# Optimization experiments

Hardware: AMD Instinct MI355X
Metric: run time of the kernel (lower is better)

Reference implementation:

```python
import jax, jax.numpy as jnp
import numpy as np

B, S, D_IN, D_INT, D_OUT, E, K_SYN = 2, 2048, 2048, 2048, 2048, 4, 512
GROUPS = D_INT // 8  # Conv1d groups

def setup_inputs() -> dict:
    key = jax.random.key(0)
    ks = jax.random.split(key, 20)
    n = lambda k, sh, std: jax.random.normal(k, sh, dtype=jnp.float32) * std
    d = {}
    d['x'] = jax.random.normal(ks[0], (B, S, D_IN), dtype=jnp.float32)
    d['syntax_ids'] = jax.random.randint(ks[1], (B, S), 0, K_SYN, dtype=jnp.int32)
    d['W_in'] = n(ks[2], (D_IN, D_INT), D_IN ** -0.5)
    d['b_in'] = jnp.zeros((D_INT,), jnp.float32)
    d['W_syn_emb'] = n(ks[3], (K_SYN, D_INT // 4), 0.02)
    d['W_syn'] = n(ks[4], (D_INT + D_INT // 4, D_INT), 0.02)
    d['b_syn'] = jnp.zeros((D_INT,), jnp.float32)
    d['W_gate'] = n(ks[5], (D_INT, 1), 0.02)
    d['b_gate'] = jnp.zeros((1,), jnp.float32)
    d['W_router'] = n(ks[6], (D_INT, E), 0.02)
    d['b_router'] = jnp.zeros((E,), jnp.float32)
    d['W_e1'] = n(ks[7], (E, D_INT, 2 * D_INT), 0.02)
    d['b_e1'] = jnp.zeros((E, 2 * D_INT), jnp.float32)
    d['W_e2'] = n(ks[8], (E, 2 * D_INT, D_INT), 0.02)
    d['b_e2'] = jnp.zeros((E, D_INT), jnp.float32)
    d['W_ctx'] = n(ks[9], (D_INT, D_INT), D_INT ** -0.5)
    d['b_ctx'] = jnp.zeros((D_INT,), jnp.float32)
    fan = 8 * 3 + 8 * 3
    lim = float(np.sqrt(6.0 / fan))
    d['conv_w'] = jax.random.uniform(ks[10], (D_INT, 8, 3), jnp.float32, -lim, lim)
    d['conv_b'] = jnp.zeros((D_INT,), jnp.float32)
    d['W_out'] = n(ks[11], (D_INT, D_OUT), D_INT ** -0.5)
    d['b_out'] = jnp.zeros((D_OUT,), jnp.float32)
    return d

def _forward(x, syntax_ids, W_in, b_in, W_syn_emb, W_syn, b_syn, W_gate, b_gate,
             W_router, b_router, W_e1, b_e1, W_e2, b_e2, W_ctx, b_ctx,
             conv_w, conv_b, W_out, b_out):
    # input projection + SiLU (dropout is identity in eval / p=0)
    h = jax.nn.silu(jnp.einsum('bsi,id->bsd', x, W_in) + b_in)
    # syntax-aware projection
    se = W_syn_emb[syntax_ids]                       # [B,S,D/4] gather
    h = jnp.einsum('bsc,cd->bsd', jnp.concatenate([h, se], axis=-1), W_syn) + b_syn
    # adaptive computation gate
    gate = jax.nn.sigmoid(jnp.einsum('bsd,do->bso', h, W_gate) + b_gate)
    h = h * gate
    # dense mixture-of-experts combine (softmax router weights)
    probs = jax.nn.softmax(jnp.einsum('bsd,de->bse', h, W_router) + b_router, axis=-1)
    eh = jax.nn.silu(jnp.einsum('bsd,edf->bsef', h, W_e1) + b_e1)   # [B,S,E,2D]
    eo = jnp.einsum('bsef,efd->bsed', eh, W_e2) + b_e2              # [B,S,E,D]
    h = h + jnp.einsum('bsed,bse->bsd', eo, probs)
    # code-specific: context linear + grouped Conv1d pattern extractor
    ctx = jnp.einsum('bsd,df->bsf', h, W_ctx) + b_ctx
    hc = jnp.transpose(h, (0, 2, 1))  # [B,D,S]
    pat = jax.lax.conv_general_dilated(
        hc, conv_w, window_strides=(1,), padding=((1, 1),),
        dimension_numbers=('NCH', 'OIH', 'NCH'), feature_group_count=GROUPS)
    pat = jnp.transpose(pat + conv_b[None, :, None], (0, 2, 1))
    h = h + ctx + pat
    out = jnp.einsum('bsd,do->bso', h, W_out) + b_out
    return out + x  # residual (input_dim == output_dim)

def reference(x, syntax_ids, W_in, b_in, W_syn_emb, W_syn, b_syn, W_gate, b_gate,
              W_router, b_router, W_e1, b_e1, W_e2, b_e2, W_ctx, b_ctx,
              conv_w, conv_b, W_out, b_out):
    return _forward(x, syntax_ids, W_in, b_in, W_syn_emb, W_syn, b_syn, W_gate,
                    b_gate, W_router, b_router, W_e1, b_e1, W_e2, b_e2,
                    W_ctx, b_ctx, conv_w, conv_b, W_out, b_out)
```

## Files before the change

kernel.cpp:

```cpp
#include <hip/hip_runtime.h>

typedef __attribute__((ext_vector_type(8))) short short8;
typedef __attribute__((ext_vector_type(4))) float floatx4;

#define BM 128
#define BN 128
#define BK 32

__device__ __forceinline__ float b2f(ushort us) {
    union { unsigned u; float f; } v; v.u = ((unsigned)us) << 16; return v.f;
}
__device__ __forceinline__ ushort f2b(float f) {
    union { float f; unsigned u; } v; v.f = f;
    unsigned r = (v.u + 0x7fffu + ((v.u >> 16) & 1u)) >> 16;
    return (ushort)r;
}
__device__ __forceinline__ float ldany(const void* p, long i, int bf) {
    return bf ? b2f(((const ushort*)p)[i]) : ((const float*)p)[i];
}
__device__ __forceinline__ void async16(const ushort* g, ushort* l) {
    __builtin_amdgcn_global_load_lds((const __attribute__((address_space(1))) void*)g,
                                     (__attribute__((address_space(3))) void*)l,
                                     16, 0, 0);
}

__global__ void detect_dtype(const unsigned* __restrict__ w, int* __restrict__ flag)
{
    if (threadIdx.x == 0 && blockIdx.x == 0) {
        int votes = 0;
        for (int i = 0; i < 256; i++) {
            unsigned e = (w[i] >> 7) & 0xFFu;
            if (e >= 112u && e <= 128u) votes++;
        }
        *flag = (votes >= 128) ? 1 : 0;
    }
}

__global__ __launch_bounds__(256) void transpose_any(
    const void* __restrict__ in, long in_off, ushort* __restrict__ out,
    int R, int C, const int* __restrict__ flag)
{
    __shared__ float tile[64][65];
    const int bf = *flag;
    const int t  = threadIdx.x;
    const long r0 = (long)blockIdx.y * 64;
    const long c0 = (long)blockIdx.x * 64;
    const int rl = t >> 4;
    const int cl = (t & 15) * 4;
    #pragma unroll
    for (int p = 0; p < 4; p++) {
        const int r = rl + p * 16;
        const long base = in_off + (r0 + r) * C + c0 + cl;
        if (bf) {
            ushort4 v = *(const ushort4*)((const ushort*)in + base);
            tile[r][cl + 0] = b2f(v.x); tile[r][cl + 1] = b2f(v.y);
            tile[r][cl + 2] = b2f(v.z); tile[r][cl + 3] = b2f(v.w);
        } else {
            float4 v = *(const float4*)((const float*)in + base);
            tile[r][cl + 0] = v.x; tile[r][cl + 1] = v.y;
            tile[r][cl + 2] = v.z; tile[r][cl + 3] = v.w;
        }
    }
    __syncthreads();
    #pragma unroll
    for (int p = 0; p < 4; p++) {
        const int oc = rl + p * 16;
        ushort4 v;
        v.x = f2b(tile[cl + 0][oc]); v.y = f2b(tile[cl + 1][oc]);
        v.z = f2b(tile[cl + 2][oc]); v.w = f2b(tile[cl + 3][oc]);
        *(ushort4*)(out + (c0 + oc) * R + r0 + cl) = v;
    }
}

__global__ void to_bf16_any(const void* __restrict__ in, ushort* __restrict__ out,
                            long n4, const int* __restrict__ flag)
{
    const long i = (long)blockIdx.x * blockDim.x + threadIdx.x;
    if (i >= n4) return;
    const int bf = *flag;
    ushort4 o;
    if (bf) {
        o = ((const ushort4*)in)[i];
    } else {
        float4 v = ((const float4*)in)[i];
        o.x = f2b(v.x); o.y = f2b(v.y); o.z = f2b(v.z); o.w = f2b(v.w);
    }
    ((ushort4*)out)[i] = o;
}

__global__ void f32_to_bf16_4(const float* __restrict__ in, ushort* __restrict__ out, long n4)
{
    const long i = (long)blockIdx.x * blockDim.x + threadIdx.x;
    if (i >= n4) return;
    float4 v = ((const float4*)in)[i];
    ushort4 o; o.x = f2b(v.x); o.y = f2b(v.y); o.z = f2b(v.z); o.w = f2b(v.w);
    ((ushort4*)out)[i] = o;
}

#define EPI_SILU   0
#define EPI_BIAS   1
#define EPI_EXPERT 2
#define EPI_CTX    3
#define EPI_OUT    4

template<int EPI>
__global__ __launch_bounds__(256, 2) void gemm_bt(
    const ushort* __restrict__ A, const ushort* __restrict__ Bt,
    int M, int N, int K,
    const void* __restrict__ bias, long bias_off,
    void* __restrict__ out, long ldo,
    float* __restrict__ hacc,
    const float* __restrict__ rowscale,
    const ushort* __restrict__ resid,
    const int* __restrict__ flag)
{
    __shared__ __align__(16) ushort As[BM * BK];
    __shared__ __align__(16) ushort Bs[BN * BK];

    const int tid  = threadIdx.x;
    const int lane = tid & 63;
    const int wv   = tid >> 6;
    const int wm   = wv & 1;
    const int wn   = wv >> 1;
    const long m0  = (long)blockIdx.y * BM;
    const long n0  = (long)blockIdx.x * BN;

    floatx4 acc[4][4] = {};

    const int sr = (lane >> 2);
    const int sk = (lane & 3) * 8;
    const ushort* Ag = A  + (m0 + wv * 32 + sr) * (long)K + sk;
    const ushort* Bg = Bt + (n0 + wv * 32 + sr) * (long)K + sk;
    ushort* Al = As + (wv * 32) * BK;
    ushort* Bl = Bs + (wv * 32) * BK;

    const int fr = lane & 15;
    const int q  = lane >> 4;
    const ushort* ApL = As + (wm * 64 + fr) * BK + q * 8;
    const ushort* BpL = Bs + (wn * 64 + fr) * BK + q * 8;

    for (int k0 = 0; k0 < K; k0 += BK) {
        __syncthreads();
        async16(Ag + k0,            Al);
        async16(Ag + 16L * K + k0,  Al + 16 * BK);
        async16(Bg + k0,            Bl);
        async16(Bg + 16L * K + k0,  Bl + 16 * BK);
        __syncthreads();
        short8 af[4], bfr[4];
        #pragma unroll
        for (int i = 0; i < 4; i++) af[i]  = *(const short8*)(ApL + i * 16 * BK);
        #pragma unroll
        for (int j = 0; j < 4; j++) bfr[j] = *(const short8*)(BpL + j * 16 * BK);
        #pragma unroll
        for (int i = 0; i < 4; i++)
            #pragma unroll
            for (int j = 0; j < 4; j++)
                acc[i][j] = __builtin_amdgcn_mfma_f32_16x16x32_bf16(
                                af[i], bfr[j], acc[i][j], 0, 0, 0);
    }

    const int bf = *flag;
    #pragma unroll
    for (int i = 0; i < 4; i++) {
        #pragma unroll
        for (int r = 0; r < 4; r++) {
            const long m = m0 + wm * 64 + i * 16 + q * 4 + r;
            #pragma unroll
            for (int j = 0; j < 4; j++) {
                const long n = n0 + wn * 64 + j * 16 + fr;
                float v = acc[i][j][r] + ldany(bias, bias_off + n, bf);
                if (EPI == EPI_SILU) {
                    v = v / (1.f + __expf(-v));
                    ((ushort*)out)[m * ldo + n] = f2b(v);
                } else if (EPI == EPI_BIAS) {
                    ((ushort*)out)[m * ldo + n] = f2b(v);
                } else if (EPI == EPI_EXPERT) {
                    hacc[m * (long)N + n] += rowscale[m * 4] * v;
                } else if (EPI == EPI_CTX) {
                    hacc[m * (long)N + n] += v;
                } else {
                    v += b2f(resid[m * (long)N + n]);
                    if (bf) ((ushort*)out)[m * ldo + n] = f2b(v);
                    else    ((float*)out)[m * ldo + n]  = v;
                }
            }
        }
    }
}

__global__ void gather_syn(const int* __restrict__ ids, const void* __restrict__ emb,
                           ushort* __restrict__ hA, const int* __restrict__ flag)
{
    const int bf = *flag;
    const long m = blockIdx.x;
    const int id = ids[m];
    const int j = threadIdx.x * 2;
    float a, b;
    if (bf) {
        ushort2 v = *(const ushort2*)((const ushort*)emb + (long)id * 512 + j);
        a = b2f(v.x); b = b2f(v.y);
    } else {
        float2 v = *(const float2*)((const float*)emb + (long)id * 512 + j);
        a = v.x; b = v.y;
    }
    ushort2 o; o.x = f2b(a); o.y = f2b(b);
    *(ushort2*)(hA + m * 2560 + 2048 + j) = o;
}

__global__ __launch_bounds__(256) void gate_router(
    ushort* __restrict__ h2, float* __restrict__ hacc, float* __restrict__ probs,
    const void* __restrict__ Wg, const void* __restrict__ bg,
    const void* __restrict__ Wr, const void* __restrict__ br,
    const int* __restrict__ flag)
{
    const int bf = *flag;
    const long m = blockIdx.x;
    const int t = threadIdx.x;
    const int lane = t & 63;
    const int wv = t >> 6;
    ushort* row = h2 + m * 2048;

    float sg = 0.f, s0 = 0.f, s1 = 0.f, s2 = 0.f, s3 = 0.f;
    for (int k = t; k < 2048; k += 256) {
        const float h = b2f(row[k]);
        sg += h * ldany(Wg, k, bf);
        float r0v, r1v, r2v, r3v;
        if (bf) {
            ushort4 v = *(const ushort4*)((const ushort*)Wr + (long)k * 4);
            r0v = b2f(v.x); r1v = b2f(v.y); r2v = b2f(v.z); r3v = b2f(v.w);
        } else {
            float4 v = *(const float4*)((const float*)Wr + (long)k * 4);
            r0v = v.x; r1v = v.y; r2v = v.z; r3v = v.w;
        }
        s0 += h * r0v; s1 += h * r1v; s2 += h * r2v; s3 += h * r3v;
    }
    #pragma unroll
    for (int off = 32; off > 0; off >>= 1) {
        sg += __shfl_down(sg, off);
        s0 += __shfl_down(s0, off);
        s1 += __shfl_down(s1, off);
        s2 += __shfl_down(s2, off);
        s3 += __shfl_down(s3, off);
    }
    __shared__ float red[4][5];
    __shared__ float gate_bc;
    if (lane == 0) {
        red[wv][0] = sg; red[wv][1] = s0; red[wv][2] = s1;
        red[wv][3] = s2; red[wv][4] = s3;
    }
    __syncthreads();
    if (t == 0) {
        float G = red[0][0] + red[1][0] + red[2][0] + red[3][0];
        float R[4];
        #pragma unroll
        for (int e = 0; e < 4; e++)
            R[e] = red[0][1 + e] + red[1][1 + e] + red[2][1 + e] + red[3][1 + e];
        const float gate = 1.f / (1.f + __expf(-(G + ldany(bg, 0, bf))));
        float lg[4], mx = -1e30f;
        #pragma unroll
        for (int e = 0; e < 4; e++) {
            lg[e] = gate * R[e] + ldany(br, e, bf);
            mx = fmaxf(mx, lg[e]);
        }
        float p[4], s = 0.f;
        #pragma unroll
        for (int e = 0; e < 4; e++) { p[e] = __expf(lg[e] - mx); s += p[e]; }
        #pragma unroll
        for (int e = 0; e < 4; e++) probs[m * 4 + e] = p[e] / s;
        gate_bc = gate;
    }
    __syncthreads();
    const float gate = gate_bc;
    for (int k = t; k < 2048; k += 256) {
        const float v = b2f(row[k]) * gate;
        row[k] = f2b(v);
        hacc[m * 2048 + k] = v;
    }
}

__global__ __launch_bounds__(256) void conv_combine(
    const ushort* __restrict__ h4, const float* __restrict__ hacc,
    const void* __restrict__ cw, const void* __restrict__ cb,
    ushort* __restrict__ h5, const int* __restrict__ flag)
{
    const int S = 2048, D = 2048;
    const int bf = *flag;
    const int b = blockIdx.z, g = blockIdx.y;
    const int s0 = blockIdx.x * 64;
    __shared__ float tile[66 * 8];
    const int t = threadIdx.x;
    for (int idx = t; idx < 66 * 8; idx += 256) {
        const int sl = idx >> 3, i = idx & 7;
        const int s = s0 + sl - 1;
        float v = 0.f;
        if (s >= 0 && s < S) v = b2f(h4[((long)b * S + s) * D + g * 8 + i]);
        tile[idx] = v;
    }
    __syncthreads();
    const int io = t & 7;
    const int c = g * 8 + io;
    float w[3][8];
    #pragma unroll
    for (int kk = 0; kk < 3; kk++)
        #pragma unroll
        for (int ii = 0; ii < 8; ii++)
            w[kk][ii] = ldany(cw, (long)c * 24 + ii * 3 + kk, bf);
    const float bc = ldany(cb, c, bf);
    #pragma unroll
    for (int p = 0; p < 2; p++) {
        const int sl = (t >> 3) + p * 32;
        float pat = 0.f;
        #pragma unroll
        for (int kk = 0; kk < 3; kk++)
            #pragma unroll
            for (int ii = 0; ii < 8; ii++)
                pat += tile[(sl + kk) * 8 + ii] * w[kk][ii];
        const long m = (long)b * S + s0 + sl;
        h5[m * D + c] = f2b(hacc[m * D + c] + bc + pat);
    }
}

extern "C" void kernel_launch(void* const* d_in, const int* in_sizes, int n_in,
                              void* d_out, int out_size, void* d_ws, size_t ws_size,
                              hipStream_t stream)
{
    (void)in_sizes; (void)n_in; (void)out_size; (void)ws_size;
    const void* x        = d_in[0];
    const int*  syn      = (const int*)d_in[1];
    const void* W_in     = d_in[2];
    const void* b_in     = d_in[3];
    const void* W_synemb = d_in[4];
    const void* W_syn    = d_in[5];
    const void* b_syn    = d_in[6];
    const void* W_gate   = d_in[7];
    const void* b_gate   = d_in[8];
    const void* W_router = d_in[9];
    const void* b_router = d_in[10];
    const void* W_e1     = d_in[11];
    const void* b_e1     = d_in[12];
    const void* W_e2     = d_in[13];
    const void* b_e2     = d_in[14];
    const void* W_ctx    = d_in[15];
    const void* b_ctx    = d_in[16];
    const void* conv_w   = d_in[17];
    const void* conv_b   = d_in[18];
    const void* W_out    = d_in[19];
    const void* b_out    = d_in[20];

    char* ws = (char*)d_ws;
    int*    flag  = (int*)ws;
    ushort* WT    = (ushort*)(ws + 256);
    ushort* xb    = (ushort*)(ws + 16777472);
    ushort* hA    = (ushort*)(ws + 33554688);
    ushort* eh    = (ushort*)(ws + 16777472);
    ushort* h23   = (ushort*)(ws + 54526208);
    float*  probs = (float*)(ws + 71303424);
    float*  hacc  = (float*)(ws + 71368960);
    const int M = 4096;
    dim3 blk(256);

    detect_dtype<<<dim3(1), dim3(64), 0, stream>>>((const unsigned*)W_in, flag);
    to_bf16_any<<<dim3(8192), blk, 0, stream>>>(x, xb, 2097152L, flag);

    transpose_any<<<dim3(32, 32), blk, 0, stream>>>(W_in, 0, WT, 2048, 2048, flag);
    gemm_bt<EPI_SILU><<<dim3(16, 32), blk, 0, stream>>>(
        xb, WT, M, 2048, 2048, b_in, 0, hA, 2560, nullptr, nullptr, nullptr, flag);
    gather_syn<<<dim3(4096), blk, 0, stream>>>(syn, W_synemb, hA, flag);
    transpose_any<<<dim3(32, 40), blk, 0, stream>>>(W_syn, 0, WT, 2560, 2048, flag);
    gemm_bt<EPI_BIAS><<<dim3(16, 32), blk, 0, stream>>>(
        hA, WT, M, 2048, 2560, b_syn, 0, h23, 2048, nullptr, nullptr, nullptr, flag);
    gate_router<<<dim3(4096), blk, 0, stream>>>(
        h23, hacc, probs, W_gate, b_gate, W_router, b_router, flag);
    for (int e = 0; e < 4; e++) {
        transpose_any<<<dim3(64, 32), blk, 0, stream>>>(
            W_e1, (long)e * 8388608, WT, 2048, 4096, flag);
        gemm_bt<EPI_SILU><<<dim3(32, 32), blk, 0, stream>>>(
            h23, WT, M, 4096, 2048, b_e1, (long)e * 4096, eh, 4096,
            nullptr, nullptr, nullptr, flag);
        transpose_any<<<dim3(32, 64), blk, 0, stream>>>(
            W_e2, (long)e * 8388608, WT, 4096, 2048, flag);
        gemm_bt<EPI_EXPERT><<<dim3(16, 32), blk, 0, stream>>>(
            eh, WT, M, 2048, 4096, b_e2, (long)e * 2048, nullptr, 0,
            hacc, probs + e, nullptr, flag);
    }
    to_bf16_any<<<dim3(8192), blk, 0, stream>>>(x, xb, 2097152L, flag);
    f32_to_bf16_4<<<dim3(8192), blk, 0, stream>>>(hacc, h23, 2097152L);
    transpose_any<<<dim3(32, 32), blk, 0, stream>>>(W_ctx, 0, WT, 2048, 2048, flag);
    gemm_bt<EPI_CTX><<<dim3(16, 32), blk, 0, stream>>>(
        h23, WT, M, 2048, 2048, b_ctx, 0, nullptr, 0, hacc, nullptr, nullptr, flag);
    conv_combine<<<dim3(32, 256, 2), blk, 0, stream>>>(
        h23, hacc, conv_w, conv_b, hA, flag);
    transpose_any<<<dim3(32, 32), blk, 0, stream>>>(W_out, 0, WT, 2048, 2048, flag);
    gemm_bt<EPI_OUT><<<dim3(16, 32), blk, 0, stream>>>(
        hA, WT, M, 2048, 2048, b_out, 0, d_out, 2048, nullptr, nullptr, xb, flag);
}
```

Baseline: 1.562 ms.

## Replace GEMM with 8-wave double-buffered ping-pong MFMA kernel using swizzled LDS

```diff
diff --git a/kernel.cpp b/kernel.cpp
--- a/kernel.cpp
+++ b/kernel.cpp
@@ -2,10 +2,6 @@
 
 typedef __attribute__((ext_vector_type(8))) short short8;
 typedef __attribute__((ext_vector_type(4))) float floatx4;
-
-#define BM 128
-#define BN 128
-#define BK 32
 
 __device__ __forceinline__ float b2f(ushort us) {
     union { unsigned u; float f; } v; v.u = ((unsigned)us) << 16; return v.f;
@@ -103,8 +99,74 @@
 #define EPI_CTX    3
 #define EPI_OUT    4
 
-template<int EPI>
-__global__ __launch_bounds__(256, 2) void gemm_bt(
+#define BAR()        __builtin_amdgcn_s_barrier()
+#define WAIT_LGKM0() asm volatile("s_waitcnt lgkmcnt(0)" ::: "memory")
+#define WAIT_VM6()   asm volatile("s_waitcnt vmcnt(6)" ::: "memory")
+#define WAIT_VM5()   asm volatile("s_waitcnt vmcnt(5)" ::: "memory")
+#define WAIT_VM0()   asm volatile("s_waitcnt vmcnt(0)" ::: "memory")
+
+#define STAGE_A(BUF, H, KT) do {                                               \
+    const long _k0 = (long)(KT) << 6;                                          \
+    _Pragma("unroll")                                                          \
+    for (int _i = 0; _i < AINSTR; ++_i) {                                      \
+        const int _gi   = w + _i * 8;                                          \
+        const int _s    = _gi / AHALF_GRP;                                     \
+        const int _wg   = _gi % AHALF_GRP;                                     \
+        const int _row0 = _s * (BM / 2) + (H) * (BM / 4) + _wg * 8;            \
+        const int _grow = _row0 + (lane >> 3);                                 \
+        async16(A + (m0 + _grow) * (long)K + _k0 +                             \
+                    (((lane & 7) ^ (_grow & 7)) << 3),                         \
+                smem + (BUF) * BUFU + _row0 * 64);                             \
+    } } while (0)
+
+#define STAGE_B(BUF, H, KT) do {                                               \
+    const long _k0 = (long)(KT) << 6;                                          \
+    _Pragma("unroll")                                                          \
+    for (int _i = 0; _i < 2; ++_i) {                                           \
+        const int _gi   = w * 2 + _i;                                          \
+        const int _row0 = (_gi >> 2) * 64 + (H) * 32 + (_gi & 3) * 8;          \
+        const int _grow = _row0 + (lane >> 3);                                 \
+        async16(Bt + (n0 + _grow) * (long)K + _k0 +                            \
+                     (((lane & 7) ^ (_grow & 7)) << 3),                        \
+                smem + (BUF) * BUFU + BM * 64 + _row0 * 64);                   \
+    } } while (0)
+
+#define LOAD_A(BUF, MH) do {                                                   \
+    _Pragma("unroll")                                                          \
+    for (int _m = 0; _m < MF / 2; ++_m) {                                      \
+        const int _row = wm * (BM / 2) + ((MH) * (MF / 2) + _m) * 16 + fr;     \
+        _Pragma("unroll")                                                      \
+        for (int _ks = 0; _ks < 2; ++_ks)                                      \
+            a[_m][_ks] = *(const short8*)(smem + (BUF) * BUFU + _row * 64 +    \
+                                          (((_ks * 4 + q) ^ (_row & 7)) << 3));\
+    } } while (0)
+
+#define LOAD_B(BUF, NH, BREG) do {                                             \
+    _Pragma("unroll")                                                          \
+    for (int _n = 0; _n < 2; ++_n) {                                           \
+        const int _row = wn * 64 + ((NH) * 2 + _n) * 16 + fr;                  \
+        _Pragma("unroll")                                                      \
+        for (int _ks = 0; _ks < 2; ++_ks)                                      \
+            BREG[_n][_ks] = *(const short8*)(smem + (BUF) * BUFU + BM * 64 +   \
+                                             _row * 64 +                       \
+                                          (((_ks * 4 + q) ^ (_row & 7)) << 3));\
+    } } while (0)
+
+#define MMA(MH, NH, BREG) do {                                                 \
+    _Pragma("unroll")                                                          \
+    for (int _m = 0; _m < MF / 2; ++_m)                                        \
+    _Pragma("unroll")                                                          \
+    for (int _n = 0; _n < 2; ++_n)                                             \
+    _Pragma("unroll")                                                          \
+    for (int _ks = 0; _ks < 2; ++_ks)                                          \
+        acc[(MH) * (MF / 2) + _m][(NH) * 2 + _n] =                             \
+            __builtin_amdgcn_mfma_f32_16x16x32_bf16(                           \
+                a[_m][_ks], BREG[_n][_ks],                                     \
+                acc[(MH) * (MF / 2) + _m][(NH) * 2 + _n], 0, 0, 0);            \
+    } while (0)
+
+template<int EPI, int MF>
+__global__ __launch_bounds__(512, 2) void gemm8(
     const ushort* __restrict__ A, const ushort* __restrict__ Bt,
     int M, int N, int K,
     const void* __restrict__ bias, long bias_off,
@@ -114,59 +176,69 @@
     const ushort* __restrict__ resid,
     const int* __restrict__ flag)
 {
-    __shared__ __align__(16) ushort As[BM * BK];
-    __shared__ __align__(16) ushort Bs[BN * BK];
+    constexpr int BM        = MF * 32;
+    constexpr int AHALF_GRP = BM / 32;
+    constexpr int AINSTR    = BM / 128;
+    constexpr int BUFU      = (BM + 256) * 64;
+    extern __shared__ ushort smem[];
 
     const int tid  = threadIdx.x;
     const int lane = tid & 63;
-    const int wv   = tid >> 6;
-    const int wm   = wv & 1;
-    const int wn   = wv >> 1;
+    const int w    = tid >> 6;
+    const int wm   = w >> 2;
+    const int wn   = w & 3;
+    const int fr   = lane & 15;
+    const int q    = lane >> 4;
     const long m0  = (long)blockIdx.y * BM;
-    const long n0  = (long)blockIdx.x * BN;
-
-    floatx4 acc[4][4] = {};
-
-    const int sr = (lane >> 2);
-    const int sk = (lane & 3) * 8;
-    const ushort* Ag = A  + (m0 + wv * 32 + sr) * (long)K + sk;
-    const ushort* Bg = Bt + (n0 + wv * 32 + sr) * (long)K + sk;
-    ushort* Al = As + (wv * 32) * BK;
-    ushort* Bl = Bs + (wv * 32) * BK;
-
-    const int fr = lane & 15;
-    const int q  = lane >> 4;
-    const ushort* ApL = As + (wm * 64 + fr) * BK + q * 8;
-    const ushort* BpL = Bs + (wn * 64 + fr) * BK + q * 8;
-
-    for (int k0 = 0; k0 < K; k0 += BK) {
-        __syncthreads();
-        async16(Ag + k0,            Al);
-        async16(Ag + 16L * K + k0,  Al + 16 * BK);
-        async16(Bg + k0,            Bl);
-        async16(Bg + 16L * K + k0,  Bl + 16 * BK);
-        __syncthreads();
-        short8 af[4], bfr[4];
-        #pragma unroll
-        for (int i = 0; i < 4; i++) af[i]  = *(const short8*)(ApL + i * 16 * BK);
-        #pragma unroll
-        for (int j = 0; j < 4; j++) bfr[j] = *(const short8*)(BpL + j * 16 * BK);
-        #pragma unroll
-        for (int i = 0; i < 4; i++)
+    const long n0  = (long)blockIdx.x * 256;
+    const int NT   = K >> 6;
+
+    floatx4 acc[MF][4] = {};
+    short8 a[MF / 2][2];
+    short8 b0[2][2], b1[2][2];
+
+    STAGE_A(0, 0, 0); STAGE_A(0, 1, 0); STAGE_B(0, 0, 0); STAGE_B(0, 1, 0);
+    STAGE_A(1, 0, 1); STAGE_B(1, 0, 1); STAGE_B(1, 1, 1);
+    if constexpr (MF == 8) WAIT_VM6(); else WAIT_VM5();
+    BAR();
+
+    for (int t = 0; t < NT; ++t) {
+        const int cur = t & 1, nxt = cur ^ 1;
+        LOAD_A(cur, 0);
+        LOAD_B(cur, 0, b0);
+        if (t + 1 < NT) STAGE_A(nxt, 1, t + 1);
+        BAR(); WAIT_LGKM0();
+        __builtin_amdgcn_s_setprio(1); MMA(0, 0, b0); __builtin_amdgcn_s_setprio(0);
+        BAR();
+        LOAD_B(cur, 1, b1);
+        if (t + 2 < NT) STAGE_A(cur, 0, t + 2);
+        BAR(); WAIT_LGKM0();
+        __builtin_amdgcn_s_setprio(1); MMA(0, 1, b1); __builtin_amdgcn_s_setprio(0);
+        BAR();
+        LOAD_A(cur, 1);
+        if (t + 2 < NT) STAGE_B(cur, 0, t + 2);
+        BAR(); WAIT_LGKM0();
+        __builtin_amdgcn_s_setprio(1); MMA(1, 1, b1); __builtin_amdgcn_s_setprio(0);
+        BAR();
+        if (t + 2 < NT) {
+            STAGE_B(cur, 1, t + 2);
+            if constexpr (MF == 8) WAIT_VM6(); else WAIT_VM5();
+        } else {
+            WAIT_VM0();
+        }
+        BAR();
+        __builtin_amdgcn_s_setprio(1); MMA(1, 0, b0); __builtin_amdgcn_s_setprio(0);
+        BAR();
+    }
+
+    const int bf = *flag;
+    #pragma unroll
+    for (int i = 0; i < MF; ++i) {
+        #pragma unroll
+        for (int r = 0; r < 4; ++r) {
+            const long m = m0 + wm * (BM / 2) + i * 16 + q * 4 + r;
             #pragma unroll
-            for (int j = 0; j < 4; j++)
-                acc[i][j] = __builtin_amdgcn_mfma_f32_16x16x32_bf16(
-                                af[i], bfr[j], acc[i][j], 0, 0, 0);
-    }
-
-    const int bf = *flag;
-    #pragma unroll
-    for (int i = 0; i < 4; i++) {
-        #pragma unroll
-        for (int r = 0; r < 4; r++) {
-            const long m = m0 + wm * 64 + i * 16 + q * 4 + r;
-            #pragma unroll
-            for (int j = 0; j < 4; j++) {
+            for (int j = 0; j < 4; ++j) {
                 const long n = n0 + wn * 64 + j * 16 + fr;
                 float v = acc[i][j][r] + ldany(bias, bias_off + n, bf);
                 if (EPI == EPI_SILU) {
@@ -358,39 +430,58 @@
     float*  hacc  = (float*)(ws + 71368960);
     const int M = 4096;
     dim3 blk(256);
+    const int LDS4 = 98304;
+    const int LDS8 = 131072;
+
+    static bool attr_set = false;
+    if (!attr_set) {
+        (void)hipFuncSetAttribute(reinterpret_cast<const void*>(&gemm8<EPI_SILU,   4>),
+                                  hipFuncAttributeMaxDynamicSharedMemorySize, LDS4);
+        (void)hipFuncSetAttribute(reinterpret_cast<const void*>(&gemm8<EPI_BIAS,   4>),
+                                  hipFuncAttributeMaxDynamicSharedMemorySize, LDS4);
+        (void)hipFuncSetAttribute(reinterpret_cast<const void*>(&gemm8<EPI_EXPERT, 4>),
+                                  hipFuncAttributeMaxDynamicSharedMemorySize, LDS4);
+        (void)hipFuncSetAttribute(reinterpret_cast<const void*>(&gemm8<EPI_CTX,    4>),
+                                  hipFuncAttributeMaxDynamicSharedMemorySize, LDS4);
+        (void)hipFuncSetAttribute(reinterpret_cast<const void*>(&gemm8<EPI_OUT,    4>),
+                                  hipFuncAttributeMaxDynamicSharedMemorySize, LDS4);
+        (void)hipFuncSetAttribute(reinterpret_cast<const void*>(&gemm8<EPI_SILU,   8>),
+                                  hipFuncAttributeMaxDynamicSharedMemorySize, LDS8);
+        attr_set = true;
+    }
 
     detect_dtype<<<dim3(1), dim3(64), 0, stream>>>((const unsigned*)W_in, flag);
     to_bf16_any<<<dim3(8192), blk, 0, stream>>>(x, xb, 2097152L, flag);
 
     transpose_any<<<dim3(32, 32), blk, 0, stream>>>(W_in, 0, WT, 2048, 2048, flag);
-    gemm_bt<EPI_SILU><<<dim3(16, 32), blk, 0, stream>>>(
+    gemm8<EPI_SILU, 4><<<dim3(8, 32), dim3(512), LDS4, stream>>>(
         xb, WT, M, 2048, 2048, b_in, 0, hA, 2560, nullptr, nullptr, nullptr, flag);
     gather_syn<<<dim3(4096), blk, 0, stream>>>(syn, W_synemb, hA, flag);
     transpose_any<<<dim3(32, 40), blk, 0, stream>>>(W_syn, 0, WT, 2560, 2048, flag);
-    gemm_bt<EPI_BIAS><<<dim3(16, 32), blk, 0, stream>>>(
+    gemm8<EPI_BIAS, 4><<<dim3(8, 32), dim3(512), LDS4, stream>>>(
         hA, WT, M, 2048, 2560, b_syn, 0, h23, 2048, nullptr, nullptr, nullptr, flag);
     gate_router<<<dim3(4096), blk, 0, stream>>>(
         h23, hacc, probs, W_gate, b_gate, W_router, b_router, flag);
     for (int e = 0; e < 4; e++) {
         transpose_any<<<dim3(64, 32), blk, 0, stream>>>(
             W_e1, (long)e * 8388608, WT, 2048, 4096, flag);
-        gemm_bt<EPI_SILU><<<dim3(32, 32), blk, 0, stream>>>(
+        gemm8<EPI_SILU, 8><<<dim3(16, 16), dim3(512), LDS8, stream>>>(
             h23, WT, M, 4096, 2048, b_e1, (long)e * 4096, eh, 4096,
             nullptr, nullptr, nullptr, flag);
         transpose_any<<<dim3(32, 64), blk, 0, stream>>>(
             W_e2, (long)e * 8388608, WT, 4096, 2048, flag);
-        gemm_bt<EPI_EXPERT><<<dim3(16, 32), blk, 0, stream>>>(
+        gemm8<EPI_EXPERT, 4><<<dim3(8, 32), dim3(512), LDS4, stream>>>(
             eh, WT, M, 2048, 4096, b_e2, (long)e * 2048, nullptr, 0,
             hacc, probs + e, nullptr, flag);
     }
     to_bf16_any<<<dim3(8192), blk, 0, stream>>>(x, xb, 2097152L, flag);
     f32_to_bf16_4<<<dim3(8192), blk, 0, stream>>>(hacc, h23, 2097152L);
     transpose_any<<<dim3(32, 32), blk, 0, stream>>>(W_ctx, 0, WT, 2048, 2048, flag);
-    gemm_bt<EPI_CTX><<<dim3(16, 32), blk, 0, stream>>>(
+    gemm8<EPI_CTX, 4><<<dim3(8, 32), dim3(512), LDS4, stream>>>(
         h23, WT, M, 2048, 2048, b_ctx, 0, nullptr, 0, hacc, nullptr, nullptr, flag);
     conv_combine<<<dim3(32, 256, 2), blk, 0, stream>>>(
         h23, hacc, conv_w, conv_b, hA, flag);
     transpose_any<<<dim3(32, 32), blk, 0, stream>>>(W_out, 0, WT, 2048, 2048, flag);
-    gemm_bt<EPI_OUT><<<dim3(16, 32), blk, 0, stream>>>(
+    gemm8<EPI_OUT, 4><<<dim3(8, 32), dim3(512), LDS4, stream>>>(
         hA, WT, M, 2048, 2048, b_out, 0, d_out, 2048, nullptr, nullptr, xb, flag);
 }
```

Measured after the change: 1.469 ms. -6.0%, faster.
